# Optimization experiments

Measured on AMD Instinct MI355X. Metric: run time of the kernel, lower is better.

Reference implementation:

```python
import jax, jax.numpy as jnp
import numpy as np

NUM_EXPERTS = 8
HIDDEN = 2048
INTER = 1408
TOKENS = 2048
TOP_K = 2


def setup_inputs() -> dict:
    key = jax.random.key(0)
    ks = jax.random.split(key, 6)
    s_h = 1.0 / np.sqrt(HIDDEN)
    s_i = 1.0 / np.sqrt(INTER)
    hidden_states = jax.random.normal(ks[0], (TOKENS, HIDDEN), dtype=jnp.float32)
    top_k_index = jax.random.randint(ks[1], (TOKENS, TOP_K), 0, NUM_EXPERTS)
    w = jax.random.uniform(ks[2], (TOKENS, TOP_K), dtype=jnp.float32)
    top_k_weights = w / jnp.sum(w, axis=-1, keepdims=True)
    # weights stored as [E, in, out] for einsum (torch Linear is [out, in])
    gate_w = jax.random.uniform(ks[3], (NUM_EXPERTS, HIDDEN, INTER), jnp.float32, -s_h, s_h)
    up_w = jax.random.uniform(ks[4], (NUM_EXPERTS, HIDDEN, INTER), jnp.float32, -s_h, s_h)
    down_w = jax.random.uniform(ks[5], (NUM_EXPERTS, INTER, HIDDEN), jnp.float32, -s_i, s_i)
    return {
        "hidden_states": hidden_states,
        "top_k_index": top_k_index,
        "top_k_weights": top_k_weights,
        "gate_w": gate_w,
        "up_w": up_w,
        "down_w": down_w,
    }


def reference(hidden_states, top_k_index, top_k_weights, gate_w, up_w, down_w):
    # combine weight per (expert, token): w_et = sum_k topk_w[t,k] * [idx[t,k]==e]
    one_hot = jax.nn.one_hot(top_k_index, NUM_EXPERTS, dtype=hidden_states.dtype)  # [T,K,E]
    combine = jnp.einsum("tk,tke->et", top_k_weights, one_hot)  # [E,T]
    # dense per-expert SwiGLU MLP over all tokens (mask-combine form of the
    # gather/scatter loop; identical math since combine weight is 0 for
    # non-routed (expert, token) pairs)
    g = jnp.einsum("th,ehi->eti", hidden_states, gate_w)  # [E,T,I]
    u = jnp.einsum("th,ehi->eti", hidden_states, up_w)
    y = jnp.einsum("eti,eih->eth", jax.nn.silu(g) * u, down_w)  # [E,T,H]
    out = jnp.einsum("et,eth->th", combine, y)  # [T,H]
    return out
```

## Files before the change

kernel.cpp:

```cpp
#include <hip/hip_runtime.h>
#include <cstdint>
#include <cstddef>

#define NE 8
#define HD 2048
#define IN 1408
#define NT 2048
#define NP (NT*2)
#define MAXMT 40

typedef __bf16 bf16;
typedef __bf16 bf16x8 __attribute__((ext_vector_type(8)));
typedef __bf16 bf16x4 __attribute__((ext_vector_type(4)));
typedef float f32x4 __attribute__((ext_vector_type(4)));

__device__ __forceinline__ void load_lds16(const void* g, void* l) {
  __builtin_amdgcn_global_load_lds((const __attribute__((address_space(1))) uint32_t*)g,
                                   (__attribute__((address_space(3))) uint32_t*)l, 16, 0, 0);
}

__global__ void k_cvt(const float* __restrict__ x, bf16* __restrict__ y) {
  int i = blockIdx.x * 256 + threadIdx.x;
  f32x4 v = ((const f32x4*)x)[i];
  bf16x4 o;
  o[0] = (bf16)v[0]; o[1] = (bf16)v[1]; o[2] = (bf16)v[2]; o[3] = (bf16)v[3];
  ((bf16x4*)y)[i] = o;
}

__global__ void k_route(const int* __restrict__ idx, const float* __restrict__ w,
                        int* __restrict__ perm_tok, float* __restrict__ perm_w,
                        int* __restrict__ slot_of, int* __restrict__ tiles) {
  __shared__ int cnt[NE], off[NE + 1], rk[NE];
  int tid = threadIdx.x;
  if (tid < NE) { cnt[tid] = 0; rk[tid] = 0; }
  __syncthreads();
  for (int a = tid; a < NP; a += 256) atomicAdd(&cnt[idx[a]], 1);
  __syncthreads();
  if (tid == 0) { off[0] = 0; for (int e = 0; e < NE; e++) off[e + 1] = off[e] + cnt[e]; }
  __syncthreads();
  for (int a = tid; a < NP; a += 256) {
    int e = idx[a];
    int p = off[e] + atomicAdd(&rk[e], 1);
    perm_tok[p] = a >> 1;
    perm_w[p] = w[a];
    slot_of[a] = p;
  }
  __syncthreads();
  if (tid == 0) {
    int n = 0;
    for (int e = 0; e < NE; e++)
      for (int r = off[e]; r < off[e + 1]; r += 128) {
        tiles[n] = e; tiles[MAXMT + n] = r; tiles[2 * MAXMT + n] = off[e + 1];
        n++;
      }
    for (int s = n; s < MAXMT; s++) tiles[s] = -1;
  }
}

__launch_bounds__(256, 2)
__global__ void k_gemm1(const bf16* __restrict__ hid, const float* __restrict__ gw,
                        const float* __restrict__ uw, const int* __restrict__ perm_tok,
                        const float* __restrict__ perm_w, const int* __restrict__ tiles,
                        bf16* __restrict__ act) {
  int b = blockIdx.x;
  int q = b >> 5, r5 = b & 31;
  int p = q * 8 + (r5 & 7);
  if (p >= 110) return;
  int slot = (p / 11) * 4 + (r5 >> 3);
  int e = tiles[slot];
  if (e < 0) return;
  int nt = p % 11;
  int row0 = tiles[MAXMT + slot], rowend = tiles[2 * MAXMT + slot];
  int nb = nt * 128;

  __shared__ bf16 As[128 * 64];
  __shared__ bf16 Bg[128 * 64];
  __shared__ bf16 Bu[128 * 64];

  int tid = threadIdx.x;
  int lane = tid & 63, wave = tid >> 6;
  int wm = (wave >> 1) * 64, wn = (wave & 1) * 64;

  const bf16* aG[4]; bf16* aL[4];
#pragma unroll
  for (int i2 = 0; i2 < 4; i2++) {
    int s = i2 * 256 + tid;
    int r = s >> 3, c = (s & 7) ^ (r & 7);
    int tr = row0 + r; if (tr > NP - 1) tr = NP - 1;
    aG[i2] = hid + (size_t)perm_tok[tr] * HD + c * 8;
    aL[i2] = As + s * 8;
  }
  int kk = (tid & 7) * 8, nn = (tid >> 3) * 4;
  const float* gB = gw + (size_t)e * HD * IN + (size_t)kk * IN + (nb + nn);
  const float* uB = uw + (size_t)e * HD * IN + (size_t)kk * IN + (nb + nn);
  int bslot[4];
#pragma unroll
  for (int i2 = 0; i2 < 4; i2++) { int n = nn + i2; bslot[i2] = (n * 8 + ((tid & 7) ^ (n & 7))) * 8; }

  f32x4 accG[4][4] = {};
  f32x4 accU[4][4] = {};

  for (int k0 = 0; k0 < HD; k0 += 64) {
    __syncthreads();
#pragma unroll
    for (int i2 = 0; i2 < 4; i2++) load_lds16(aG[i2] + k0, aL[i2]);
    {
      f32x4 v[8];
#pragma unroll
      for (int j = 0; j < 8; j++) v[j] = *(const f32x4*)(gB + (size_t)(k0 + j) * IN);
#pragma unroll
      for (int i2 = 0; i2 < 4; i2++) {
        bf16x8 o;
#pragma unroll
        for (int j = 0; j < 8; j++) o[j] = (bf16)v[j][i2];
        *(bf16x8*)(Bg + bslot[i2]) = o;
      }
#pragma unroll
      for (int j = 0; j < 8; j++) v[j] = *(const f32x4*)(uB + (size_t)(k0 + j) * IN);
#pragma unroll
      for (int i2 = 0; i2 < 4; i2++) {
        bf16x8 o;
#pragma unroll
        for (int j = 0; j < 8; j++) o[j] = (bf16)v[j][i2];
        *(bf16x8*)(Bu + bslot[i2]) = o;
      }
    }
    __syncthreads();
#pragma unroll
    for (int ks = 0; ks < 2; ks++) {
      int ckf = ks * 4 + (lane >> 4);
      bf16x8 af[4], bgf[4], buf[4];
#pragma unroll
      for (int fm = 0; fm < 4; fm++) {
        int m = wm + fm * 16 + (lane & 15);
        af[fm] = *(const bf16x8*)(As + (m * 8 + (ckf ^ (m & 7))) * 8);
      }
#pragma unroll
      for (int fn = 0; fn < 4; fn++) {
        int n = wn + fn * 16 + (lane & 15);
        int sl = (n * 8 + (ckf ^ (n & 7))) * 8;
        bgf[fn] = *(const bf16x8*)(Bg + sl);
        buf[fn] = *(const bf16x8*)(Bu + sl);
      }
#pragma unroll
      for (int fm = 0; fm < 4; fm++)
#pragma unroll
        for (int fn = 0; fn < 4; fn++) {
          accG[fm][fn] = __builtin_amdgcn_mfma_f32_16x16x32_bf16(af[fm], bgf[fn], accG[fm][fn], 0, 0, 0);
          accU[fm][fn] = __builtin_amdgcn_mfma_f32_16x16x32_bf16(af[fm], buf[fn], accU[fm][fn], 0, 0, 0);
        }
    }
  }
#pragma unroll
  for (int fm = 0; fm < 4; fm++) {
#pragma unroll
    for (int rr = 0; rr < 4; rr++) {
      int m = wm + fm * 16 + ((lane >> 4) << 2) + rr;
      int row = row0 + m;
      if (row < rowend) {
        float pw = perm_w[row];
#pragma unroll
        for (int fn = 0; fn < 4; fn++) {
          int n = nb + wn + fn * 16 + (lane & 15);
          float g = accG[fm][fn][rr], u = accU[fm][fn][rr];
          float sv = g / (1.0f + __expf(-g));
          act[(size_t)row * IN + n] = (bf16)(sv * u * pw);
        }
      }
    }
  }
}

__launch_bounds__(256, 2)
__global__ void k_gemm2(const bf16* __restrict__ act, const float* __restrict__ dw,
                        const int* __restrict__ tiles, float* __restrict__ pout) {
  int b = blockIdx.x;
  int q = b >> 5, r5 = b & 31;
  int p = q * 8 + (r5 & 7);
  int slot = (p >> 4) * 4 + (r5 >> 3);
  int e = tiles[slot];
  if (e < 0) return;
  int nt = p & 15;
  int row0 = tiles[MAXMT + slot], rowend = tiles[2 * MAXMT + slot];
  int nb = nt * 128;

  __shared__ bf16 As[128 * 64];
  __shared__ bf16 Bd[128 * 64];

  int tid = threadIdx.x;
  int lane = tid & 63, wave = tid >> 6;
  int wm = (wave >> 1) * 64, wn = (wave & 1) * 64;

  const bf16* aG[4]; bf16* aL[4];
#pragma unroll
  for (int i2 = 0; i2 < 4; i2++) {
    int s = i2 * 256 + tid;
    int r = s >> 3, c = (s & 7) ^ (r & 7);
    int ar = row0 + r; if (ar > NP - 1) ar = NP - 1;
    aG[i2] = act + (size_t)ar * IN + c * 8;
    aL[i2] = As + s * 8;
  }
  int kk = (tid & 7) * 8, nn = (tid >> 3) * 4;
  const float* dB = dw + (size_t)e * IN * HD + (size_t)kk * HD + (nb + nn);
  int bslot[4];
#pragma unroll
  for (int i2 = 0; i2 < 4; i2++) { int n = nn + i2; bslot[i2] = (n * 8 + ((tid & 7) ^ (n & 7))) * 8; }

  f32x4 acc[4][4] = {};

  for (int k0 = 0; k0 < IN; k0 += 64) {
    __syncthreads();
#pragma unroll
    for (int i2 = 0; i2 < 4; i2++) load_lds16(aG[i2] + k0, aL[i2]);
    {
      f32x4 v[8];
#pragma unroll
      for (int j = 0; j < 8; j++) v[j] = *(const f32x4*)(dB + (size_t)(k0 + j) * HD);
#pragma unroll
      for (int i2 = 0; i2 < 4; i2++) {
        bf16x8 o;
#pragma unroll
        for (int j = 0; j < 8; j++) o[j] = (bf16)v[j][i2];
        *(bf16x8*)(Bd + bslot[i2]) = o;
      }
    }
    __syncthreads();
#pragma unroll
    for (int ks = 0; ks < 2; ks++) {
      int ckf = ks * 4 + (lane >> 4);
      bf16x8 af[4], bdf[4];
#pragma unroll
      for (int fm = 0; fm < 4; fm++) {
        int m = wm + fm * 16 + (lane & 15);
        af[fm] = *(const bf16x8*)(As + (m * 8 + (ckf ^ (m & 7))) * 8);
      }
#pragma unroll
      for (int fn = 0; fn < 4; fn++) {
        int n = wn + fn * 16 + (lane & 15);
        bdf[fn] = *(const bf16x8*)(Bd + (n * 8 + (ckf ^ (n & 7))) * 8);
      }
#pragma unroll
      for (int fm = 0; fm < 4; fm++)
#pragma unroll
        for (int fn = 0; fn < 4; fn++)
          acc[fm][fn] = __builtin_amdgcn_mfma_f32_16x16x32_bf16(af[fm], bdf[fn], acc[fm][fn], 0, 0, 0);
    }
  }
#pragma unroll
  for (int fm = 0; fm < 4; fm++) {
#pragma unroll
    for (int rr = 0; rr < 4; rr++) {
      int m = wm + fm * 16 + ((lane >> 4) << 2) + rr;
      int row = row0 + m;
      if (row < rowend) {
#pragma unroll
        for (int fn = 0; fn < 4; fn++) {
          int n = nb + wn + fn * 16 + (lane & 15);
          pout[(size_t)row * HD + n] = acc[fm][fn][rr];
        }
      }
    }
  }
}

__global__ void k_comb(const float* __restrict__ pout, const int* __restrict__ slot_of,
                       float* __restrict__ out) {
  int i = blockIdx.x * 256 + threadIdx.x;
  int t = i >> 9;
  int hc = i & 511;
  f32x4 a = ((const f32x4*)(pout + (size_t)slot_of[2 * t] * HD))[hc];
  f32x4 c = ((const f32x4*)(pout + (size_t)slot_of[2 * t + 1] * HD))[hc];
  ((f32x4*)(out + (size_t)t * HD))[hc] = a + c;
}

extern "C" void kernel_launch(void* const* d_in, const int* in_sizes, int n_in,
                              void* d_out, int out_size, void* d_ws, size_t ws_size,
                              hipStream_t stream) {
  const float* hidden  = (const float*)d_in[0];
  const int*   tk_idx  = (const int*)d_in[1];
  const float* tk_w    = (const float*)d_in[2];
  const float* gw      = (const float*)d_in[3];
  const float* uw      = (const float*)d_in[4];
  const float* dw      = (const float*)d_in[5];
  float* out = (float*)d_out;

  char* ws = (char*)d_ws;
  int*   perm_tok = (int*)ws;
  float* perm_w   = (float*)(ws + 16384);
  int*   slot_of  = (int*)(ws + 32768);
  int*   tiles    = (int*)(ws + 49152);
  bf16*  hid_bf   = (bf16*)(ws + 53248);
  bf16*  act      = (bf16*)(ws + 53248 + 8388608);
  float* pout     = (float*)(ws + 53248 + 8388608 + 11534336);

  k_cvt  <<<4096, 256, 0, stream>>>(hidden, hid_bf);
  k_route<<<1,    256, 0, stream>>>(tk_idx, tk_w, perm_tok, perm_w, slot_of, tiles);
  k_gemm1<<<448,  256, 0, stream>>>(hid_bf, gw, uw, perm_tok, perm_w, tiles, act);
  k_gemm2<<<640,  256, 0, stream>>>(act, dw, tiles, pout);
  k_comb <<<4096, 256, 0, stream>>>(pout, slot_of, out);
}
```

Before: 481.8 us.

## Software-pipeline both MoE GEMMs with register-prefetched weights and double-buffered A tile

```diff
diff --git a/kernel.cpp b/kernel.cpp
--- a/kernel.cpp
+++ b/kernel.cpp
@@ -73,7 +73,7 @@
   int row0 = tiles[MAXMT + slot], rowend = tiles[2 * MAXMT + slot];
   int nb = nt * 128;
 
-  __shared__ bf16 As[128 * 64];
+  __shared__ bf16 As[2][128 * 64];
   __shared__ bf16 Bg[128 * 64];
   __shared__ bf16 Bu[128 * 64];
 
@@ -81,14 +81,14 @@
   int lane = tid & 63, wave = tid >> 6;
   int wm = (wave >> 1) * 64, wn = (wave & 1) * 64;
 
-  const bf16* aG[4]; bf16* aL[4];
+  const bf16* aG[4]; int aS[4];
 #pragma unroll
   for (int i2 = 0; i2 < 4; i2++) {
     int s = i2 * 256 + tid;
     int r = s >> 3, c = (s & 7) ^ (r & 7);
     int tr = row0 + r; if (tr > NP - 1) tr = NP - 1;
     aG[i2] = hid + (size_t)perm_tok[tr] * HD + c * 8;
-    aL[i2] = As + s * 8;
+    aS[i2] = s * 8;
   }
   int kk = (tid & 7) * 8, nn = (tid >> 3) * 4;
   const float* gB = gw + (size_t)e * HD * IN + (size_t)kk * IN + (nb + nn);
@@ -99,33 +99,42 @@
 
   f32x4 accG[4][4] = {};
   f32x4 accU[4][4] = {};
-
+  f32x4 vg[8], vu[8];
+
+#pragma unroll
+  for (int i2 = 0; i2 < 4; i2++) load_lds16(aG[i2], &As[0][aS[i2]]);
+#pragma unroll
+  for (int j = 0; j < 8; j++) vg[j] = *(const f32x4*)(gB + (size_t)j * IN);
+#pragma unroll
+  for (int j = 0; j < 8; j++) vu[j] = *(const f32x4*)(uB + (size_t)j * IN);
+#pragma unroll
+  for (int i2 = 0; i2 < 4; i2++) {
+    bf16x8 o;
+#pragma unroll
+    for (int j = 0; j < 8; j++) o[j] = (bf16)vg[j][i2];
+    *(bf16x8*)(Bg + bslot[i2]) = o;
+  }
+#pragma unroll
+  for (int i2 = 0; i2 < 4; i2++) {
+    bf16x8 o;
+#pragma unroll
+    for (int j = 0; j < 8; j++) o[j] = (bf16)vu[j][i2];
+    *(bf16x8*)(Bu + bslot[i2]) = o;
+  }
+  __syncthreads();
+
+  int cur = 0;
   for (int k0 = 0; k0 < HD; k0 += 64) {
-    __syncthreads();
-#pragma unroll
-    for (int i2 = 0; i2 < 4; i2++) load_lds16(aG[i2] + k0, aL[i2]);
-    {
-      f32x4 v[8];
-#pragma unroll
-      for (int j = 0; j < 8; j++) v[j] = *(const f32x4*)(gB + (size_t)(k0 + j) * IN);
-#pragma unroll
-      for (int i2 = 0; i2 < 4; i2++) {
-        bf16x8 o;
-#pragma unroll
-        for (int j = 0; j < 8; j++) o[j] = (bf16)v[j][i2];
-        *(bf16x8*)(Bg + bslot[i2]) = o;
-      }
-#pragma unroll
-      for (int j = 0; j < 8; j++) v[j] = *(const f32x4*)(uB + (size_t)(k0 + j) * IN);
-#pragma unroll
-      for (int i2 = 0; i2 < 4; i2++) {
-        bf16x8 o;
-#pragma unroll
-        for (int j = 0; j < 8; j++) o[j] = (bf16)v[j][i2];
-        *(bf16x8*)(Bu + bslot[i2]) = o;
-      }
-    }
-    __syncthreads();
+    int nxt = k0 + 64;
+    if (nxt < HD) {
+#pragma unroll
+      for (int i2 = 0; i2 < 4; i2++) load_lds16(aG[i2] + nxt, &As[cur ^ 1][aS[i2]]);
+#pragma unroll
+      for (int j = 0; j < 8; j++) vg[j] = *(const f32x4*)(gB + (size_t)(nxt + j) * IN);
+#pragma unroll
+      for (int j = 0; j < 8; j++) vu[j] = *(const f32x4*)(uB + (size_t)(nxt + j) * IN);
+    }
+    const bf16* Ac = As[cur];
 #pragma unroll
     for (int ks = 0; ks < 2; ks++) {
       int ckf = ks * 4 + (lane >> 4);
@@ -133,7 +142,7 @@
 #pragma unroll
       for (int fm = 0; fm < 4; fm++) {
         int m = wm + fm * 16 + (lane & 15);
-        af[fm] = *(const bf16x8*)(As + (m * 8 + (ckf ^ (m & 7))) * 8);
+        af[fm] = *(const bf16x8*)(Ac + (m * 8 + (ckf ^ (m & 7))) * 8);
       }
 #pragma unroll
       for (int fn = 0; fn < 4; fn++) {
@@ -149,6 +158,25 @@
           accG[fm][fn] = __builtin_amdgcn_mfma_f32_16x16x32_bf16(af[fm], bgf[fn], accG[fm][fn], 0, 0, 0);
           accU[fm][fn] = __builtin_amdgcn_mfma_f32_16x16x32_bf16(af[fm], buf[fn], accU[fm][fn], 0, 0, 0);
         }
+    }
+    __syncthreads();
+    if (nxt < HD) {
+#pragma unroll
+      for (int i2 = 0; i2 < 4; i2++) {
+        bf16x8 o;
+#pragma unroll
+        for (int j = 0; j < 8; j++) o[j] = (bf16)vg[j][i2];
+        *(bf16x8*)(Bg + bslot[i2]) = o;
+      }
+#pragma unroll
+      for (int i2 = 0; i2 < 4; i2++) {
+        bf16x8 o;
+#pragma unroll
+        for (int j = 0; j < 8; j++) o[j] = (bf16)vu[j][i2];
+        *(bf16x8*)(Bu + bslot[i2]) = o;
+      }
+      cur ^= 1;
+      __syncthreads();
     }
   }
 #pragma unroll
@@ -184,21 +212,21 @@
   int row0 = tiles[MAXMT + slot], rowend = tiles[2 * MAXMT + slot];
   int nb = nt * 128;
 
-  __shared__ bf16 As[128 * 64];
+  __shared__ bf16 As[2][128 * 64];
   __shared__ bf16 Bd[128 * 64];
 
   int tid = threadIdx.x;
   int lane = tid & 63, wave = tid >> 6;
   int wm = (wave >> 1) * 64, wn = (wave & 1) * 64;
 
-  const bf16* aG[4]; bf16* aL[4];
+  const bf16* aG[4]; int aS[4];
 #pragma unroll
   for (int i2 = 0; i2 < 4; i2++) {
     int s = i2 * 256 + tid;
     int r = s >> 3, c = (s & 7) ^ (r & 7);
     int ar = row0 + r; if (ar > NP - 1) ar = NP - 1;
     aG[i2] = act + (size_t)ar * IN + c * 8;
-    aL[i2] = As + s * 8;
+    aS[i2] = s * 8;
   }
   int kk = (tid & 7) * 8, nn = (tid >> 3) * 4;
   const float* dB = dw + (size_t)e * IN * HD + (size_t)kk * HD + (nb + nn);
@@ -207,24 +235,31 @@
   for (int i2 = 0; i2 < 4; i2++) { int n = nn + i2; bslot[i2] = (n * 8 + ((tid & 7) ^ (n & 7))) * 8; }
 
   f32x4 acc[4][4] = {};
-
+  f32x4 vd[8];
+
+#pragma unroll
+  for (int i2 = 0; i2 < 4; i2++) load_lds16(aG[i2], &As[0][aS[i2]]);
+#pragma unroll
+  for (int j = 0; j < 8; j++) vd[j] = *(const f32x4*)(dB + (size_t)j * HD);
+#pragma unroll
+  for (int i2 = 0; i2 < 4; i2++) {
+    bf16x8 o;
+#pragma unroll
+    for (int j = 0; j < 8; j++) o[j] = (bf16)vd[j][i2];
+    *(bf16x8*)(Bd + bslot[i2]) = o;
+  }
+  __syncthreads();
+
+  int cur = 0;
   for (int k0 = 0; k0 < IN; k0 += 64) {
-    __syncthreads();
-#pragma unroll
-    for (int i2 = 0; i2 < 4; i2++) load_lds16(aG[i2] + k0, aL[i2]);
-    {
-      f32x4 v[8];
-#pragma unroll
-      for (int j = 0; j < 8; j++) v[j] = *(const f32x4*)(dB + (size_t)(k0 + j) * HD);
-#pragma unroll
-      for (int i2 = 0; i2 < 4; i2++) {
-        bf16x8 o;
-#pragma unroll
-        for (int j = 0; j < 8; j++) o[j] = (bf16)v[j][i2];
-        *(bf16x8*)(Bd + bslot[i2]) = o;
-      }
-    }
-    __syncthreads();
+    int nxt = k0 + 64;
+    if (nxt < IN) {
+#pragma unroll
+      for (int i2 = 0; i2 < 4; i2++) load_lds16(aG[i2] + nxt, &As[cur ^ 1][aS[i2]]);
+#pragma unroll
+      for (int j = 0; j < 8; j++) vd[j] = *(const f32x4*)(dB + (size_t)(nxt + j) * HD);
+    }
+    const bf16* Ac = As[cur];
 #pragma unroll
     for (int ks = 0; ks < 2; ks++) {
       int ckf = ks * 4 + (lane >> 4);
@@ -232,7 +267,7 @@
 #pragma unroll
       for (int fm = 0; fm < 4; fm++) {
         int m = wm + fm * 16 + (lane & 15);
-        af[fm] = *(const bf16x8*)(As + (m * 8 + (ckf ^ (m & 7))) * 8);
+        af[fm] = *(const bf16x8*)(Ac + (m * 8 + (ckf ^ (m & 7))) * 8);
       }
 #pragma unroll
       for (int fn = 0; fn < 4; fn++) {
@@ -244,6 +279,18 @@
 #pragma unroll
         for (int fn = 0; fn < 4; fn++)
           acc[fm][fn] = __builtin_amdgcn_mfma_f32_16x16x32_bf16(af[fm], bdf[fn], acc[fm][fn], 0, 0, 0);
+    }
+    __syncthreads();
+    if (nxt < IN) {
+#pragma unroll
+      for (int i2 = 0; i2 < 4; i2++) {
+        bf16x8 o;
+#pragma unroll
+        for (int j = 0; j < 8; j++) o[j] = (bf16)vd[j][i2];
+        *(bf16x8*)(Bd + bslot[i2]) = o;
+      }
+      cur ^= 1;
+      __syncthreads();
     }
   }
 #pragma unroll
```

Result: slower. 511.6 us (+6.2%).

## Halve GEMM M-tile to 64 rows and raise occupancy in expert GEMMs

Applied to the files above, without the earlier changes.

```diff
diff --git a/kernel.cpp b/kernel.cpp
--- a/kernel.cpp
+++ b/kernel.cpp
@@ -7,7 +7,7 @@
 #define IN 1408
 #define NT 2048
 #define NP (NT*2)
-#define MAXMT 40
+#define MAXMT 72
 
 typedef __bf16 bf16;
 typedef __bf16 bf16x8 __attribute__((ext_vector_type(8)));
@@ -49,7 +49,7 @@
   if (tid == 0) {
     int n = 0;
     for (int e = 0; e < NE; e++)
-      for (int r = off[e]; r < off[e + 1]; r += 128) {
+      for (int r = off[e]; r < off[e + 1]; r += 64) {
         tiles[n] = e; tiles[MAXMT + n] = r; tiles[2 * MAXMT + n] = off[e + 1];
         n++;
       }
@@ -57,38 +57,34 @@
   }
 }
 
-__launch_bounds__(256, 2)
+__launch_bounds__(256, 3)
 __global__ void k_gemm1(const bf16* __restrict__ hid, const float* __restrict__ gw,
                         const float* __restrict__ uw, const int* __restrict__ perm_tok,
                         const float* __restrict__ perm_w, const int* __restrict__ tiles,
                         bf16* __restrict__ act) {
-  int b = blockIdx.x;
-  int q = b >> 5, r5 = b & 31;
-  int p = q * 8 + (r5 & 7);
-  if (p >= 110) return;
-  int slot = (p / 11) * 4 + (r5 >> 3);
+  int w = blockIdx.x;
+  int slot = w / 11, nt = w % 11;
   int e = tiles[slot];
   if (e < 0) return;
-  int nt = p % 11;
   int row0 = tiles[MAXMT + slot], rowend = tiles[2 * MAXMT + slot];
   int nb = nt * 128;
 
-  __shared__ bf16 As[128 * 64];
+  __shared__ bf16 As[64 * 64];
   __shared__ bf16 Bg[128 * 64];
   __shared__ bf16 Bu[128 * 64];
 
   int tid = threadIdx.x;
   int lane = tid & 63, wave = tid >> 6;
-  int wm = (wave >> 1) * 64, wn = (wave & 1) * 64;
-
-  const bf16* aG[4]; bf16* aL[4];
-#pragma unroll
-  for (int i2 = 0; i2 < 4; i2++) {
+  int wm = (wave >> 1) * 32, wn = (wave & 1) * 64;
+
+  const bf16* aG[2]; int aS[2];
+#pragma unroll
+  for (int i2 = 0; i2 < 2; i2++) {
     int s = i2 * 256 + tid;
     int r = s >> 3, c = (s & 7) ^ (r & 7);
     int tr = row0 + r; if (tr > NP - 1) tr = NP - 1;
     aG[i2] = hid + (size_t)perm_tok[tr] * HD + c * 8;
-    aL[i2] = As + s * 8;
+    aS[i2] = s * 8;
   }
   int kk = (tid & 7) * 8, nn = (tid >> 3) * 4;
   const float* gB = gw + (size_t)e * HD * IN + (size_t)kk * IN + (nb + nn);
@@ -97,13 +93,13 @@
 #pragma unroll
   for (int i2 = 0; i2 < 4; i2++) { int n = nn + i2; bslot[i2] = (n * 8 + ((tid & 7) ^ (n & 7))) * 8; }
 
-  f32x4 accG[4][4] = {};
-  f32x4 accU[4][4] = {};
+  f32x4 accG[2][4] = {};
+  f32x4 accU[2][4] = {};
 
   for (int k0 = 0; k0 < HD; k0 += 64) {
     __syncthreads();
 #pragma unroll
-    for (int i2 = 0; i2 < 4; i2++) load_lds16(aG[i2] + k0, aL[i2]);
+    for (int i2 = 0; i2 < 2; i2++) load_lds16(aG[i2] + k0, &As[aS[i2]]);
     {
       f32x4 v[8];
 #pragma unroll
@@ -129,9 +125,9 @@
 #pragma unroll
     for (int ks = 0; ks < 2; ks++) {
       int ckf = ks * 4 + (lane >> 4);
-      bf16x8 af[4], bgf[4], buf[4];
-#pragma unroll
-      for (int fm = 0; fm < 4; fm++) {
+      bf16x8 af[2], bgf[4], buf[4];
+#pragma unroll
+      for (int fm = 0; fm < 2; fm++) {
         int m = wm + fm * 16 + (lane & 15);
         af[fm] = *(const bf16x8*)(As + (m * 8 + (ckf ^ (m & 7))) * 8);
       }
@@ -143,7 +139,7 @@
         buf[fn] = *(const bf16x8*)(Bu + sl);
       }
 #pragma unroll
-      for (int fm = 0; fm < 4; fm++)
+      for (int fm = 0; fm < 2; fm++)
 #pragma unroll
         for (int fn = 0; fn < 4; fn++) {
           accG[fm][fn] = __builtin_amdgcn_mfma_f32_16x16x32_bf16(af[fm], bgf[fn], accG[fm][fn], 0, 0, 0);
@@ -152,7 +148,7 @@
     }
   }
 #pragma unroll
-  for (int fm = 0; fm < 4; fm++) {
+  for (int fm = 0; fm < 2; fm++) {
 #pragma unroll
     for (int rr = 0; rr < 4; rr++) {
       int m = wm + fm * 16 + ((lane >> 4) << 2) + rr;
@@ -171,34 +167,31 @@
   }
 }
 
-__launch_bounds__(256, 2)
+__launch_bounds__(256, 4)
 __global__ void k_gemm2(const bf16* __restrict__ act, const float* __restrict__ dw,
                         const int* __restrict__ tiles, float* __restrict__ pout) {
-  int b = blockIdx.x;
-  int q = b >> 5, r5 = b & 31;
-  int p = q * 8 + (r5 & 7);
-  int slot = (p >> 4) * 4 + (r5 >> 3);
+  int w = blockIdx.x;
+  int slot = w >> 4, nt = w & 15;
   int e = tiles[slot];
   if (e < 0) return;
-  int nt = p & 15;
   int row0 = tiles[MAXMT + slot], rowend = tiles[2 * MAXMT + slot];
   int nb = nt * 128;
 
-  __shared__ bf16 As[128 * 64];
+  __shared__ bf16 As[64 * 64];
   __shared__ bf16 Bd[128 * 64];
 
   int tid = threadIdx.x;
   int lane = tid & 63, wave = tid >> 6;
-  int wm = (wave >> 1) * 64, wn = (wave & 1) * 64;
-
-  const bf16* aG[4]; bf16* aL[4];
-#pragma unroll
-  for (int i2 = 0; i2 < 4; i2++) {
+  int wm = (wave >> 1) * 32, wn = (wave & 1) * 64;
+
+  const bf16* aG[2]; int aS[2];
+#pragma unroll
+  for (int i2 = 0; i2 < 2; i2++) {
     int s = i2 * 256 + tid;
     int r = s >> 3, c = (s & 7) ^ (r & 7);
     int ar = row0 + r; if (ar > NP - 1) ar = NP - 1;
     aG[i2] = act + (size_t)ar * IN + c * 8;
-    aL[i2] = As + s * 8;
+    aS[i2] = s * 8;
   }
   int kk = (tid & 7) * 8, nn = (tid >> 3) * 4;
   const float* dB = dw + (size_t)e * IN * HD + (size_t)kk * HD + (nb + nn);
@@ -206,12 +199,12 @@
 #pragma unroll
   for (int i2 = 0; i2 < 4; i2++) { int n = nn + i2; bslot[i2] = (n * 8 + ((tid & 7) ^ (n & 7))) * 8; }
 
-  f32x4 acc[4][4] = {};
+  f32x4 acc[2][4] = {};
 
   for (int k0 = 0; k0 < IN; k0 += 64) {
     __syncthreads();
 #pragma unroll
-    for (int i2 = 0; i2 < 4; i2++) load_lds16(aG[i2] + k0, aL[i2]);
+    for (int i2 = 0; i2 < 2; i2++) load_lds16(aG[i2] + k0, &As[aS[i2]]);
     {
       f32x4 v[8];
 #pragma unroll
@@ -228,9 +221,9 @@
 #pragma unroll
     for (int ks = 0; ks < 2; ks++) {
       int ckf = ks * 4 + (lane >> 4);
-      bf16x8 af[4], bdf[4];
-#pragma unroll
-      for (int fm = 0; fm < 4; fm++) {
+      bf16x8 af[2], bdf[4];
+#pragma unroll
+      for (int fm = 0; fm < 2; fm++) {
         int m = wm + fm * 16 + (lane & 15);
         af[fm] = *(const bf16x8*)(As + (m * 8 + (ckf ^ (m & 7))) * 8);
       }
@@ -240,14 +233,14 @@
         bdf[fn] = *(const bf16x8*)(Bd + (n * 8 + (ckf ^ (n & 7))) * 8);
       }
 #pragma unroll
-      for (int fm = 0; fm < 4; fm++)
+      for (int fm = 0; fm < 2; fm++)
 #pragma unroll
         for (int fn = 0; fn < 4; fn++)
           acc[fm][fn] = __builtin_amdgcn_mfma_f32_16x16x32_bf16(af[fm], bdf[fn], acc[fm][fn], 0, 0, 0);
     }
   }
 #pragma unroll
-  for (int fm = 0; fm < 4; fm++) {
+  for (int fm = 0; fm < 2; fm++) {
 #pragma unroll
     for (int rr = 0; rr < 4; rr++) {
       int m = wm + fm * 16 + ((lane >> 4) << 2) + rr;
@@ -293,9 +286,9 @@
   bf16*  act      = (bf16*)(ws + 53248 + 8388608);
   float* pout     = (float*)(ws + 53248 + 8388608 + 11534336);
 
-  k_cvt  <<<4096, 256, 0, stream>>>(hidden, hid_bf);
-  k_route<<<1,    256, 0, stream>>>(tk_idx, tk_w, perm_tok, perm_w, slot_of, tiles);
-  k_gemm1<<<448,  256, 0, stream>>>(hid_bf, gw, uw, perm_tok, perm_w, tiles, act);
-  k_gemm2<<<640,  256, 0, stream>>>(act, dw, tiles, pout);
-  k_comb <<<4096, 256, 0, stream>>>(pout, slot_of, out);
-}
+  k_cvt  <<<4096,     256, 0, stream>>>(hidden, hid_bf);
+  k_route<<<1,        256, 0, stream>>>(tk_idx, tk_w, perm_tok, perm_w, slot_of, tiles);
+  k_gemm1<<<MAXMT*11, 256, 0, stream>>>(hid_bf, gw, uw, perm_tok, perm_w, tiles, act);
+  k_gemm2<<<MAXMT*16, 256, 0, stream>>>(act, dw, tiles, pout);
+  k_comb <<<4096,     256, 0, stream>>>(pout, slot_of, out);
+}
```

New measurement: 561.8 us. 16.6% more time.
